# Performance work log

Hardware: AMD Instinct MI355X
Metric: run time of the kernel (lower is better)

Reference implementation:

```python
import jax, jax.numpy as jnp
import numpy as np

NUM_GRAPHS = 64

def _mlp(x, Wa, ba, Wb, bb):
    # 2-layer MLP: Linear -> ReLU -> Linear
    return jnp.maximum(x @ Wa + ba, 0.0) @ Wb + bb

def setup_inputs() -> dict:
    key = jax.random.key(0)
    ks = jax.random.split(key, 16)
    N1, E1, N2, E2 = 20000, 640000, 640000, 1280000
    d_x1, d_x2, d_e2, d_h, d_et, d_out = 32, 32, 16, 64, 32, 32
    inp = {
        'x1': jax.random.normal(ks[0], (N1, d_x1), jnp.float32),
        'x2': jax.random.normal(ks[1], (N2, d_x2), jnp.float32),
        'edge_index1': jax.random.randint(ks[2], (2, E1), 0, N1),
        'edge_index2': jax.random.randint(ks[3], (2, E2), 0, N2),
        'x1_batch': jnp.sort(jax.random.randint(ks[4], (N1,), 0, NUM_GRAPHS)),
        'edge_attr2': jax.random.normal(ks[5], (E2, d_e2), jnp.float32),
        # mlp2 (DGCN edge network): in = d_x2 + d_e2 = 48 -> 64 -> 32
        'W2a': jax.random.normal(ks[6], (d_x2 + d_e2, d_h), jnp.float32) * 0.05,
        'b2a': jnp.zeros((d_h,), jnp.float32),
        'W2b': jax.random.normal(ks[7], (d_h, d_et), jnp.float32) * 0.05,
        'b2b': jnp.zeros((d_et,), jnp.float32),
        # mlp (MOLGCN edge-conditioned network): in = d_x1 + d_et = 64 -> 64 -> 32
        'W1a': jax.random.normal(ks[8], (d_x1 + d_et, d_h), jnp.float32) * 0.05,
        'b1a': jnp.zeros((d_h,), jnp.float32),
        'W1b': jax.random.normal(ks[9], (d_h, d_out), jnp.float32) * 0.05,
        'b1b': jnp.zeros((d_out,), jnp.float32),
    }
    return inp

def reference(x1, x2, edge_index1, edge_index2, x1_batch, edge_attr2,
              W2a, b2a, W2b, b2b, W1a, b1a, W1b, b1b):
    N1, N2 = x1.shape[0], x2.shape[0]
    # --- DGCN over graph 2: message = mlp2([x_src, edge_attr]), sum-aggregate at dst ---
    s2, d2 = edge_index2[0], edge_index2[1]
    msg2 = _mlp(jnp.concatenate([x2[s2], edge_attr2], axis=-1), W2a, b2a, W2b, b2b)  # [E2, d_et]
    e_t = jax.ops.segment_sum(msg2, d2, num_segments=N2)  # [N2, d_et]; N2 == E1 (line graph)
    # --- MOLGCN over graph 1: edge-conditioned message = mlp([x_src, e_t]), sum at dst ---
    s1, d1 = edge_index1[0], edge_index1[1]
    msg1 = _mlp(jnp.concatenate([x1[s1], e_t], axis=-1), W1a, b1a, W1b, b1b)  # [E1, d_out]
    h = jax.ops.segment_sum(msg1, d1, num_segments=N1)  # [N1, d_out]
    # --- global add pool over graphs, then squeeze()/2 ---
    pooled = jax.ops.segment_sum(h, x1_batch, num_segments=NUM_GRAPHS)  # [G, d_out]
    return jnp.squeeze(pooled) / 2.0
```

## Files before the change

kernel.cpp:

```cpp
#include <hip/hip_runtime.h>
#include <hip/hip_bf16.h>


#define NUM_GRAPHS 64
#define CAP 4608
#define CURSTRIDE 16
#define EPB 8192
#define NCVT 2048

typedef __attribute__((ext_vector_type(8))) short bf16x8;
typedef __attribute__((ext_vector_type(4))) float f32x4;

__device__ __forceinline__ unsigned short f2bf(float x) {
    __hip_bfloat16 b = __float2bfloat16(x);
    return *(unsigned short*)&b;
}
__device__ __forceinline__ float bf2f(unsigned int u16) {
    unsigned short us = (unsigned short)u16;
    __hip_bfloat16 b = *(__hip_bfloat16*)&us;
    return __bfloat162float(b);
}
__device__ __forceinline__ unsigned int pack2(float lo, float hi) {
    return (unsigned int)f2bf(lo) | ((unsigned int)f2bf(hi) << 16);
}
__device__ __forceinline__ uint4 cvt8(const float* src) {
    const float4* s4 = (const float4*)src;
    float4 a = s4[0], b = s4[1];
    return make_uint4(pack2(a.x, a.y), pack2(a.z, a.w),
                      pack2(b.x, b.y), pack2(b.z, b.w));
}
__device__ __forceinline__ int swz(int row, int kb) {
    return row * 128 + (kb ^ ((row & 7) << 4));
}


__global__ __launch_bounds__(256) void k_prep0(
    const float* __restrict__ W2a, const float* __restrict__ b2a,
    const float* __restrict__ W2b, const float* __restrict__ b2b,
    const float* __restrict__ W1a, const float* __restrict__ b1a,
    const float* __restrict__ W1b, const float* __restrict__ b1b,
    unsigned char* __restrict__ wpack, int* __restrict__ cur, int ncur)
{
    const int tid = threadIdx.x;
    if (blockIdx.x == 0) {
        unsigned char* img1 = wpack;
        unsigned char* img2 = wpack + 12672;
        for (int i = tid; i < 64 * 64; i += 256) {
            int n = i >> 6, k = i & 63;
            float v1 = (k < 48) ? W2a[k * 64 + n] : 0.0f;
            *(unsigned short*)(img1 + n * 128 + ((2 * k) ^ ((n & 7) << 4))) = f2bf(v1);
            *(unsigned short*)(img2 + n * 128 + ((2 * k) ^ ((n & 7) << 4))) = f2bf(W1a[k * 64 + n]);
        }
        for (int i = tid; i < 32 * 64; i += 256) {
            int n = i >> 6, k = i & 63;
            *(unsigned short*)(img1 + 8192 + n * 128 + ((2 * k) ^ ((n & 7) << 4))) = f2bf(W2b[k * 32 + n]);
            *(unsigned short*)(img2 + 8192 + n * 128 + ((2 * k) ^ ((n & 7) << 4))) = f2bf(W1b[k * 32 + n]);
        }
        if (tid < 64) {
            ((float*)(img1 + 12288))[tid] = b2a[tid];
            ((float*)(img2 + 12288))[tid] = b1a[tid];
        }
        if (tid < 32) {
            ((float*)(img1 + 12544))[tid] = b2b[tid];
            ((float*)(img2 + 12544))[tid] = b1b[tid];
        }
    } else {
        for (int i = tid; i < ncur; i += 256) cur[i] = 0;
    }
}


__global__ __launch_bounds__(256) void k_bscat_cvt(
    const int* __restrict__ ei2, int E2, const int* __restrict__ ei1, int E1,
    int* __restrict__ cur, uint2* __restrict__ mid, int NB2, int NBT, int Etot, int NBB,
    const float* __restrict__ x2, uint4* __restrict__ x2b,
    const float* __restrict__ x1, uint4* __restrict__ x1b,
    const float* __restrict__ ea2, uint4* __restrict__ ea2b,
    long xn2, long xn1, long xne)
{
    __shared__ unsigned int buck[EPB];
    __shared__ int hist[512];
    __shared__ int gbase[512];
    __shared__ int wloc[512];

    const int tid = threadIdx.x;
    if (blockIdx.x >= NBB) {
        const long tot = xn2 + xn1 + xne;
        const long stride = (long)NCVT * 256;
        for (long i = (long)(blockIdx.x - NBB) * 256 + tid; i < tot; i += stride) {
            if (i < xn2) x2b[i] = cvt8(x2 + i * 8);
            else if (i < xn2 + xn1) { long j = i - xn2; x1b[j] = cvt8(x1 + j * 8); }
            else { long j = i - xn2 - xn1; ea2b[j] = cvt8(ea2 + j * 8); }
        }
        return;
    }

    const long start = (long)blockIdx.x * EPB;
    const int nloc = (int)(((long)Etot - start) < EPB ? ((long)Etot - start) : EPB);
    if (nloc <= 0) return;

    for (int i = tid; i < NBT; i += 256) hist[i] = 0;
    __syncthreads();

    for (int k = tid; k < nloc; k += 256) {
        const long i = start + k;
        int b, dlo;
        if (i < E2) {
            int d = ei2[E2 + i]; b = d >> 11; dlo = d & 2047;
        } else {
            int j = (int)(i - E2);
            int d = ei1[E1 + j]; b = NB2 + (d >> 7); dlo = d & 127;
        }
        buck[k] = (unsigned)b | ((unsigned)dlo << 16);
        atomicAdd(&hist[b], 1);
    }
    __syncthreads();

    for (int i = tid; i < NBT; i += 256) {
        const int c = hist[i];
        gbase[i] = (c > 0) ? atomicAdd(&cur[i * CURSTRIDE], c) : 0;
        wloc[i] = 0;
    }
    __syncthreads();

    for (int k = tid; k < nloc; k += 256) {
        const long i = start + k;
        const unsigned bv = buck[k];
        const int b = (int)(bv & 0xffffu), dlo = (int)(bv >> 16);
        int e, s;
        if (i < E2) { e = (int)i; s = ei2[i]; }
        else        { int j = (int)(i - E2); e = j; s = ei1[j]; }
        const int pos = gbase[b] + atomicAdd(&wloc[b], 1);
        if (pos < CAP)
            mid[(size_t)b * CAP + pos] =
                make_uint2((unsigned)e | ((unsigned)dlo << 21), (unsigned)s);
    }
}


__global__ __launch_bounds__(256) void k_csr(
    const int* __restrict__ cur, const uint2* __restrict__ mid,
    uint2* __restrict__ ord, int NB2, int E2)
{
    __shared__ int cnt[2048];
    __shared__ int cnt2[2048];
    __shared__ int red[256];
    __shared__ int wpart[4];
    __shared__ int sCarry;

    const int b = blockIdx.x, tid = threadIdx.x;
    const bool g2 = (b < NB2);
    const int span = g2 ? 2048 : 128;
    const int lo = g2 ? 0 : NB2;
    const int fill = min(cur[b * CURSTRIDE], CAP);

    int part = 0;
    for (int k = lo + tid; k < b; k += 256) part += min(cur[k * CURSTRIDE], CAP);
    red[tid] = part;
    __syncthreads();
    for (int off = 128; off >= 1; off >>= 1) {
        if (tid < off) red[tid] += red[tid + off];
        __syncthreads();
    }
    const int outBase = (g2 ? 0 : E2) + red[0];

    for (int k = tid; k < span; k += 256) cnt[k] = 0;
    __syncthreads();

    const size_t mbase = (size_t)b * CAP;
    for (int i = tid; i < fill; i += 256)
        atomicAdd(&cnt[mid[mbase + i].x >> 21], 1);
    __syncthreads();

    if (tid == 0) sCarry = 0;
    __syncthreads();
    const int lane = tid & 63, wv = tid >> 6;
    for (int c0 = 0; c0 < span; c0 += 256) {
        const int idx = c0 + tid;
        int v = (idx < span) ? cnt[idx] : 0;
        int inc = v;
        #pragma unroll
        for (int off = 1; off < 64; off <<= 1) {
            int nv = __shfl_up(inc, off, 64);
            if (lane >= off) inc += nv;
        }
        if (lane == 63) wpart[wv] = inc;
        __syncthreads();
        int wpre = 0;
        for (int wq = 0; wq < wv; ++wq) wpre += wpart[wq];
        const int excl = sCarry + wpre + inc - v;
        const int tot = wpart[0] + wpart[1] + wpart[2] + wpart[3];
        __syncthreads();
        if (idx < span) cnt[idx] = excl;
        if (tid == 0) sCarry += tot;
        __syncthreads();
    }

    for (int k = tid; k < span; k += 256) cnt2[k] = 0;
    __syncthreads();

    for (int i = tid; i < fill; i += 256) {
        uint2 r = mid[mbase + i];
        const int dl = (int)(r.x >> 21);
        const int rk = atomicAdd(&cnt2[dl], 1);
        ord[outBase + cnt[dl] + rk] = make_uint2(r.x, r.y | ((unsigned)b << 20));
    }
}


__global__ __launch_bounds__(256) void k_msg2_agg(
    const float* __restrict__ x2f, const uint4* __restrict__ x2b,
    const float* __restrict__ ea2, const uint4* __restrict__ ea2b,
    const uint2* __restrict__ ord, const unsigned char* __restrict__ wimg,
    unsigned int* __restrict__ e_t, int E, int use_bf16, int use_ea2b)
{
    __shared__ __align__(16) unsigned char sBuf[32768];
    __shared__ int sdst[257];
    __shared__ int sPrevS;
    __shared__ unsigned long long wmask[4];
    __shared__ int rstart[257];

    const int tid = threadIdx.x;
    const int base = blockIdx.x * 256, p = base + tid;

    int e = 0, s = 0, d = -1;
    if (p < E) {
        uint2 o = ord[p];
        e = (int)(o.x & 0x1FFFFFu); s = (int)(o.y & 0xFFFFFu);
        d = ((int)(o.y >> 20) << 11) + (int)(o.x >> 21);
    }
    sdst[tid] = d;
    if (tid == 0) {
        int dp = -1, dn = -1;
        if (base > 0) {
            uint2 o = ord[base - 1];
            dp = ((int)(o.y >> 20) << 11) + (int)(o.x >> 21);
        }
        if (base + 256 < E) {
            uint2 o = ord[base + 256];
            dn = ((int)(o.y >> 20) << 11) + (int)(o.x >> 21);
        }
        sPrevS = dp; sdst[256] = dn;
    }

    {
        uint4 ch[8];
        if (use_bf16) {
            const uint4* xr = x2b + (size_t)s * 4;
            #pragma unroll
            for (int c = 0; c < 4; ++c) ch[c] = xr[c];
        } else {
            const float4* xs = (const float4*)(x2f + (size_t)s * 32);
            #pragma unroll
            for (int c = 0; c < 4; ++c) {
                float4 a = xs[2 * c], b = xs[2 * c + 1];
                ch[c].x = pack2(a.x, a.y); ch[c].y = pack2(a.z, a.w);
                ch[c].z = pack2(b.x, b.y); ch[c].w = pack2(b.z, b.w);
            }
        }
        if (use_ea2b) {
            ch[4] = ea2b[(size_t)e * 2];
            ch[5] = ea2b[(size_t)e * 2 + 1];
        } else {
            const float4* es = (const float4*)(ea2 + (size_t)e * 16);
            #pragma unroll
            for (int c = 0; c < 2; ++c) {
                float4 a = es[2 * c], b = es[2 * c + 1];
                ch[4 + c].x = pack2(a.x, a.y); ch[4 + c].y = pack2(a.z, a.w);
                ch[4 + c].z = pack2(b.x, b.y); ch[4 + c].w = pack2(b.z, b.w);
            }
        }
        ch[6] = make_uint4(0, 0, 0, 0);
        ch[7] = make_uint4(0, 0, 0, 0);
        #pragma unroll
        for (int c = 0; c < 8; ++c)
            *(uint4*)(sBuf + swz(tid, c * 16)) = ch[c];
    }
    __syncthreads();

    const int lane = tid & 63, wv = tid >> 6;
    const int lr = lane & 15, lk = lane >> 4;
    const int band = wv * 64;
    const unsigned char* gWa = wimg;
    const unsigned char* gWb = wimg + 8192;
    const float* gba = (const float*)(wimg + 12288);
    const float* gbb = (const float*)(wimg + 12544);

    f32x4 accA[4][4];
    #pragma unroll
    for (int n = 0; n < 4; ++n) {
        float bv = gba[n * 16 + lr];
        #pragma unroll
        for (int m = 0; m < 4; ++m) accA[m][n] = (f32x4){bv, bv, bv, bv};
    }
    #pragma unroll
    for (int ks = 0; ks < 2; ++ks) {
        const int kb = ks * 64 + lk * 16;
        bf16x8 af[4], bfr[4];
        #pragma unroll
        for (int m = 0; m < 4; ++m)
            af[m] = *(const bf16x8*)(sBuf + swz(band + m * 16 + lr, kb));
        #pragma unroll
        for (int n = 0; n < 4; ++n) {
            int rw = n * 16 + lr;
            bfr[n] = *(const bf16x8*)(gWa + rw * 128 + (kb ^ ((rw & 7) << 4)));
        }
        #pragma unroll
        for (int m = 0; m < 4; ++m)
            #pragma unroll
            for (int n = 0; n < 4; ++n)
                accA[m][n] = __builtin_amdgcn_mfma_f32_16x16x32_bf16(af[m], bfr[n], accA[m][n], 0, 0, 0);
    }
    #pragma unroll
    for (int m = 0; m < 4; ++m)
        #pragma unroll
        for (int n = 0; n < 4; ++n)
            #pragma unroll
            for (int rr = 0; rr < 4; ++rr) {
                int grow = band + m * 16 + lk * 4 + rr;
                int cb = 2 * (n * 16 + lr);
                *(unsigned short*)(sBuf + swz(grow, cb)) = f2bf(fmaxf(accA[m][n][rr], 0.0f));
            }

    f32x4 accB[4][2];
    #pragma unroll
    for (int n = 0; n < 2; ++n) {
        float bv = gbb[n * 16 + lr];
        #pragma unroll
        for (int m = 0; m < 4; ++m) accB[m][n] = (f32x4){bv, bv, bv, bv};
    }
    #pragma unroll
    for (int ks = 0; ks < 2; ++ks) {
        const int kb = ks * 64 + lk * 16;
        bf16x8 af[4], bfr[2];
        #pragma unroll
        for (int m = 0; m < 4; ++m)
            af[m] = *(const bf16x8*)(sBuf + swz(band + m * 16 + lr, kb));
        #pragma unroll
        for (int n = 0; n < 2; ++n) {
            int rw = n * 16 + lr;
            bfr[n] = *(const bf16x8*)(gWb + rw * 128 + (kb ^ ((rw & 7) << 4)));
        }
        #pragma unroll
        for (int m = 0; m < 4; ++m)
            #pragma unroll
            for (int n = 0; n < 2; ++n)
                accB[m][n] = __builtin_amdgcn_mfma_f32_16x16x32_bf16(af[m], bfr[n], accB[m][n], 0, 0, 0);
    }
    __syncthreads();

    unsigned short* smsg = (unsigned short*)sBuf;
    #pragma unroll
    for (int m = 0; m < 4; ++m)
        #pragma unroll
        for (int n = 0; n < 2; ++n)
            #pragma unroll
            for (int rr = 0; rr < 4; ++rr)
                smsg[(band + m * 16 + lk * 4 + rr) * 33 + n * 16 + lr] = f2bf(accB[m][n][rr]);

    const bool leader = (p < E) && (tid == 0 || sdst[tid - 1] != d);
    wmask[wv] = __ballot(leader);
    __syncthreads();

    int nruns = __popcll(wmask[0]) + __popcll(wmask[1]) + __popcll(wmask[2]) + __popcll(wmask[3]);
    if (leader) {
        int before = __popcll(wmask[wv] & ((1ULL << lane) - 1));
        for (int w = 0; w < wv; ++w) before += __popcll(wmask[w]);
        rstart[before] = tid;
    }
    const int vcnt = (E - base < 256) ? (E - base) : 256;
    if (tid == 0) rstart[nruns] = vcnt;
    __syncthreads();

    const int sPrev = sPrevS;
    const int ntask = nruns * 32;
    for (int task = tid; task < ntask; task += 256) {
        const int run = task >> 5, c = task & 31;
        const int rs = rstart[run], re = rstart[run + 1];
        const int dd = sdst[rs];
        float acc = 0.0f;
        for (int qq = rs; qq < re; ++qq) acc += bf2f(smsg[qq * 33 + c]);
        const bool gs = (rs > 0) || (base == 0) || (sPrev != dd);
        const bool ge = (re < 256) || (sdst[256] != dd);
        if (gs && ge) {
            ((unsigned short*)e_t)[(size_t)dd * 32 + c] = f2bf(acc);
        } else {
            unsigned int* a32 = e_t + (size_t)dd * 16 + (c >> 1);
            const int sh = (c & 1) * 16;
            unsigned int old = *a32;
            while (true) {
                float cur2 = bf2f((old >> sh) & 0xffffu);
                unsigned int nb = f2bf(cur2 + acc);
                unsigned int nv = (old & ~(0xffffu << sh)) | (nb << sh);
                unsigned int prev = atomicCAS(a32, old, nv);
                if (prev == old) break;
                old = prev;
            }
        }
    }
}


__global__ __launch_bounds__(256) void k_msg1_agg(
    const float* __restrict__ x1f, const uint4* __restrict__ x1b,
    const unsigned int* __restrict__ e_t,
    const uint2* __restrict__ ord, const unsigned char* __restrict__ wimg,
    float* __restrict__ h, int E, int NB2, int use_bf16)
{
    __shared__ __align__(16) unsigned char sBuf[32768];
    __shared__ int sdst[257];
    __shared__ int sPrevS;
    __shared__ unsigned long long wmask[4];
    __shared__ int rstart[257];

    const int tid = threadIdx.x;
    const int base = blockIdx.x * 256, p = base + tid;

    int e = 0, s = 0, d = -1;
    if (p < E) {
        uint2 o = ord[p];
        e = (int)(o.x & 0x1FFFFFu); s = (int)(o.y & 0xFFFFFu);
        d = (((int)(o.y >> 20) - NB2) << 7) + (int)(o.x >> 21);
    }
    sdst[tid] = d;
    if (tid == 0) {
        int dp = -1, dn = -1;
        if (base > 0) {
            uint2 o = ord[base - 1];
            dp = (((int)(o.y >> 20) - NB2) << 7) + (int)(o.x >> 21);
        }
        if (base + 256 < E) {
            uint2 o = ord[base + 256];
            dn = (((int)(o.y >> 20) - NB2) << 7) + (int)(o.x >> 21);
        }
        sPrevS = dp; sdst[256] = dn;
    }

    {
        uint4 ch[8];
        if (use_bf16) {
            const uint4* xr = x1b + (size_t)s * 4;
            #pragma unroll
            for (int c = 0; c < 4; ++c) ch[c] = xr[c];
        } else {
            const float4* xs = (const float4*)(x1f + (size_t)s * 32);
            #pragma unroll
            for (int c = 0; c < 4; ++c) {
                float4 a = xs[2 * c], b = xs[2 * c + 1];
                ch[c].x = pack2(a.x, a.y); ch[c].y = pack2(a.z, a.w);
                ch[c].z = pack2(b.x, b.y); ch[c].w = pack2(b.z, b.w);
            }
        }
        const uint4* er = (const uint4*)(e_t + (size_t)e * 16);
        #pragma unroll
        for (int c = 0; c < 4; ++c) ch[4 + c] = er[c];
        #pragma unroll
        for (int c = 0; c < 8; ++c)
            *(uint4*)(sBuf + swz(tid, c * 16)) = ch[c];
    }
    __syncthreads();

    const int lane = tid & 63, wv = tid >> 6;
    const int lr = lane & 15, lk = lane >> 4;
    const int band = wv * 64;
    const unsigned char* gWa = wimg;
    const unsigned char* gWb = wimg + 8192;
    const float* gba = (const float*)(wimg + 12288);
    const float* gbb = (const float*)(wimg + 12544);

    f32x4 accA[4][4];
    #pragma unroll
    for (int n = 0; n < 4; ++n) {
        float bv = gba[n * 16 + lr];
        #pragma unroll
        for (int m = 0; m < 4; ++m) accA[m][n] = (f32x4){bv, bv, bv, bv};
    }
    #pragma unroll
    for (int ks = 0; ks < 2; ++ks) {
        const int kb = ks * 64 + lk * 16;
        bf16x8 af[4], bfr[4];
        #pragma unroll
        for (int m = 0; m < 4; ++m)
            af[m] = *(const bf16x8*)(sBuf + swz(band + m * 16 + lr, kb));
        #pragma unroll
        for (int n = 0; n < 4; ++n) {
            int rw = n * 16 + lr;
            bfr[n] = *(const bf16x8*)(gWa + rw * 128 + (kb ^ ((rw & 7) << 4)));
        }
        #pragma unroll
        for (int m = 0; m < 4; ++m)
            #pragma unroll
            for (int n = 0; n < 4; ++n)
                accA[m][n] = __builtin_amdgcn_mfma_f32_16x16x32_bf16(af[m], bfr[n], accA[m][n], 0, 0, 0);
    }
    #pragma unroll
    for (int m = 0; m < 4; ++m)
        #pragma unroll
        for (int n = 0; n < 4; ++n)
            #pragma unroll
            for (int rr = 0; rr < 4; ++rr) {
                int grow = band + m * 16 + lk * 4 + rr;
                int cb = 2 * (n * 16 + lr);
                *(unsigned short*)(sBuf + swz(grow, cb)) = f2bf(fmaxf(accA[m][n][rr], 0.0f));
            }

    f32x4 accB[4][2];
    #pragma unroll
    for (int n = 0; n < 2; ++n) {
        float bv = gbb[n * 16 + lr];
        #pragma unroll
        for (int m = 0; m < 4; ++m) accB[m][n] = (f32x4){bv, bv, bv, bv};
    }
    #pragma unroll
    for (int ks = 0; ks < 2; ++ks) {
        const int kb = ks * 64 + lk * 16;
        bf16x8 af[4], bfr[2];
        #pragma unroll
        for (int m = 0; m < 4; ++m)
            af[m] = *(const bf16x8*)(sBuf + swz(band + m * 16 + lr, kb));
        #pragma unroll
        for (int n = 0; n < 2; ++n) {
            int rw = n * 16 + lr;
            bfr[n] = *(const bf16x8*)(gWb + rw * 128 + (kb ^ ((rw & 7) << 4)));
        }
        #pragma unroll
        for (int m = 0; m < 4; ++m)
            #pragma unroll
            for (int n = 0; n < 2; ++n)
                accB[m][n] = __builtin_amdgcn_mfma_f32_16x16x32_bf16(af[m], bfr[n], accB[m][n], 0, 0, 0);
    }
    __syncthreads();

    unsigned short* smsg = (unsigned short*)sBuf;
    #pragma unroll
    for (int m = 0; m < 4; ++m)
        #pragma unroll
        for (int n = 0; n < 2; ++n)
            #pragma unroll
            for (int rr = 0; rr < 4; ++rr)
                smsg[(band + m * 16 + lk * 4 + rr) * 33 + n * 16 + lr] = f2bf(accB[m][n][rr]);

    const bool leader = (p < E) && (tid == 0 || sdst[tid - 1] != d);
    wmask[wv] = __ballot(leader);
    __syncthreads();

    int nruns = __popcll(wmask[0]) + __popcll(wmask[1]) + __popcll(wmask[2]) + __popcll(wmask[3]);
    if (leader) {
        int before = __popcll(wmask[wv] & ((1ULL << lane) - 1));
        for (int w = 0; w < wv; ++w) before += __popcll(wmask[w]);
        rstart[before] = tid;
    }
    const int vcnt = (E - base < 256) ? (E - base) : 256;
    if (tid == 0) rstart[nruns] = vcnt;
    __syncthreads();

    const int sPrev = sPrevS;
    const int ntask = nruns * 32;
    for (int task = tid; task < ntask; task += 256) {
        const int run = task >> 5, c = task & 31;
        const int rs = rstart[run], re = rstart[run + 1];
        const int dd = sdst[rs];
        float acc = 0.0f;
        for (int qq = rs; qq < re; ++qq) acc += bf2f(smsg[qq * 33 + c]);
        const bool gs = (rs > 0) || (base == 0) || (sPrev != dd);
        const bool ge = (re < 256) || (sdst[256] != dd);
        if (gs && ge) h[(size_t)dd * 32 + c] = acc;
        else atomicAdd(h + (size_t)dd * 32 + c, acc);
    }
}


__device__ __forceinline__ int lower_bound_i(const int* a, int n, int key) {
    int lo = 0, hi = n;
    while (lo < hi) {
        int mid = (lo + hi) >> 1;
        if (a[mid] < key) lo = mid + 1; else hi = mid;
    }
    return lo;
}

__global__ __launch_bounds__(256) void k_pool(const float* __restrict__ h,
                                              const int* __restrict__ batch,
                                              float* __restrict__ out, int N1) {
    const int g = blockIdx.x;
    const int lo = lower_bound_i(batch, N1, g);
    const int hi = lower_bound_i(batch, N1, g + 1);
    const int tid = threadIdx.x;
    const int c = tid & 31, rg = tid >> 5;
    float acc = 0.0f;
    for (int n = lo + rg; n < hi; n += 8) acc += h[(size_t)n * 32 + c];
    __shared__ float red[256];
    red[tid] = acc;
    __syncthreads();
    for (int off = 128; off >= 32; off >>= 1) {
        if (tid < off) red[tid] += red[tid + off];
        __syncthreads();
    }
    if (tid < 32) out[g * 32 + tid] = red[tid] * 0.5f;
}


extern "C" void kernel_launch(void* const* d_in, const int* in_sizes, int n_in,
                              void* d_out, int out_size, void* d_ws, size_t ws_size,
                              hipStream_t stream) {
    const float* x1  = (const float*)d_in[0];
    const float* x2  = (const float*)d_in[1];
    const int*   ei1 = (const int*)d_in[2];
    const int*   ei2 = (const int*)d_in[3];
    const int*   xb  = (const int*)d_in[4];
    const float* ea2 = (const float*)d_in[5];
    const float* W2a = (const float*)d_in[6];
    const float* b2a = (const float*)d_in[7];
    const float* W2b = (const float*)d_in[8];
    const float* b2b = (const float*)d_in[9];
    const float* W1a = (const float*)d_in[10];
    const float* b1a = (const float*)d_in[11];
    const float* W1b = (const float*)d_in[12];
    const float* b1b = (const float*)d_in[13];

    const int N1 = in_sizes[0] / 32;
    const int E1 = in_sizes[2] / 2;
    const int E2 = in_sizes[3] / 2;
    const int N2 = in_sizes[1] / 32;
    const int Etot = E2 + E1;

    const int NB2 = (N2 + 2047) >> 11;
    const int NB1 = (N1 + 127) >> 7;
    const int NBT = NB2 + NB1;

    const size_t sz_wpack = 25600;
    const size_t sz_cur   = (size_t)NBT * CURSTRIDE * 4;
    const size_t sz_et    = (size_t)N2 * 64;
    const size_t sz_h     = (size_t)N1 * 128;
    const size_t sz_ord   = (size_t)Etot * 8;
    const size_t sz_mid   = (size_t)NBT * CAP * 8;
    const size_t regA     = (sz_mid > sz_et + sz_h) ? sz_mid : (sz_et + sz_h);
    const size_t sz_x2b   = (size_t)N2 * 64;
    const size_t sz_x1b   = (size_t)N1 * 64;
    const size_t sz_ea2b  = (size_t)E2 * 32;
    const size_t need_x   = sz_ord + regA + sz_x2b + sz_x1b + sz_wpack + sz_cur;
    const size_t need_xe  = need_x + sz_ea2b;

    const int use_bf16 = (ws_size >= need_x) ? 1 : 0;
    const int use_ea2b = (ws_size >= need_xe) ? 1 : 0;

    char* w = (char*)d_ws;
    uint2* ord = (uint2*)w;            w += sz_ord;
    char* regionA = w;                 w += regA;
    uint4* x2b = (uint4*)w;            if (use_bf16) w += sz_x2b;
    uint4* x1b = (uint4*)w;            if (use_bf16) w += sz_x1b;
    uint4* ea2b = (uint4*)w;           if (use_ea2b) w += sz_ea2b;
    unsigned char* wpack = (unsigned char*)w;  w += sz_wpack;
    int* cur = (int*)w;

    unsigned int* e_t = (unsigned int*)regionA;
    float* h = (float*)(regionA + sz_et);
    uint2* mid = (uint2*)regionA;

    const int NBB = (Etot + EPB - 1) / EPB;
    const long xn2 = use_bf16 ? (long)N2 * 4 : 0;
    const long xn1 = use_bf16 ? (long)N1 * 4 : 0;
    const long xne = use_ea2b ? (long)E2 * 2 : 0;

    k_prep0<<<2, 256, 0, stream>>>(W2a, b2a, W2b, b2b, W1a, b1a, W1b, b1b,
                                   wpack, cur, NBT * CURSTRIDE);
    k_bscat_cvt<<<NBB + NCVT, 256, 0, stream>>>(
        ei2, E2, ei1, E1, cur, mid, NB2, NBT, Etot, NBB,
        x2, x2b, x1, x1b, ea2, ea2b, xn2, xn1, xne);
    k_csr<<<NBT, 256, 0, stream>>>(cur, mid, ord, NB2, E2);
    hipMemsetAsync(regionA, 0, sz_et + sz_h, stream);
    k_msg2_agg<<<(E2 + 255) / 256, 256, 0, stream>>>(
        x2, x2b, ea2, ea2b, ord, wpack, e_t, E2, use_bf16, use_ea2b);
    k_msg1_agg<<<(E1 + 255) / 256, 256, 0, stream>>>(
        x1, x1b, e_t, ord + E2, wpack + 12672, h, E1, NB2, use_bf16);
    k_pool<<<NUM_GRAPHS, 256, 0, stream>>>(h, xb, (float*)d_out, N1);
}
```

Measured before the change: 262.1 us.

## Carry edge-attr payload through bucket sort and renumber e_t by graph-1 edge rank

```diff
diff --git a/kernel.cpp b/kernel.cpp
--- a/kernel.cpp
+++ b/kernel.cpp
@@ -39,7 +39,8 @@
     const float* __restrict__ W2b, const float* __restrict__ b2b,
     const float* __restrict__ W1a, const float* __restrict__ b1a,
     const float* __restrict__ W1b, const float* __restrict__ b1b,
-    unsigned char* __restrict__ wpack, int* __restrict__ cur, int ncur)
+    unsigned char* __restrict__ wpack, int* __restrict__ cur, int ncur,
+    int* __restrict__ rank1, int nrank)
 {
     const int tid = threadIdx.x;
     if (blockIdx.x == 0) {
@@ -65,18 +66,24 @@
             ((float*)(img2 + 12544))[tid] = b1b[tid];
         }
     } else {
-        for (int i = tid; i < ncur; i += 256) cur[i] = 0;
+        const int Z = ncur + nrank;
+        for (int i = (blockIdx.x - 1) * 256 + tid; i < Z; i += 32 * 256) {
+            if (i < ncur) cur[i] = 0;
+            else rank1[i - ncur] = 0;
+        }
     }
 }
 
 
 __global__ __launch_bounds__(256) void k_bscat_cvt(
     const int* __restrict__ ei2, int E2, const int* __restrict__ ei1, int E1,
-    int* __restrict__ cur, uint2* __restrict__ mid, int NB2, int NBT, int Etot, int NBB,
+    int* __restrict__ cur, uint2* __restrict__ mid8,
+    uint2* __restrict__ mid2_sd, uint4* __restrict__ mid2_pay, uint2* __restrict__ mid1,
+    int NB2, int NBT, int Etot, int NBB,
     const float* __restrict__ x2, uint4* __restrict__ x2b,
     const float* __restrict__ x1, uint4* __restrict__ x1b,
     const float* __restrict__ ea2, uint4* __restrict__ ea2b,
-    long xn2, long xn1, long xne)
+    long xn2, long xn1, long xne, int use_pay)
 {
     __shared__ unsigned int buck[EPB];
     __shared__ int hist[512];
@@ -127,51 +134,33 @@
         const long i = start + k;
         const unsigned bv = buck[k];
         const int b = (int)(bv & 0xffffu), dlo = (int)(bv >> 16);
-        int e, s;
-        if (i < E2) { e = (int)i; s = ei2[i]; }
-        else        { int j = (int)(i - E2); e = j; s = ei1[j]; }
         const int pos = gbase[b] + atomicAdd(&wloc[b], 1);
-        if (pos < CAP)
-            mid[(size_t)b * CAP + pos] =
-                make_uint2((unsigned)e | ((unsigned)dlo << 21), (unsigned)s);
-    }
-}
-
-
-__global__ __launch_bounds__(256) void k_csr(
-    const int* __restrict__ cur, const uint2* __restrict__ mid,
-    uint2* __restrict__ ord, int NB2, int E2)
-{
-    __shared__ int cnt[2048];
-    __shared__ int cnt2[2048];
-    __shared__ int red[256];
+        if (pos >= CAP) continue;
+        if (i < E2) {
+            const int s = ei2[i];
+            if (use_pay) {
+                const size_t idx = (size_t)b * CAP + pos;
+                mid2_sd[idx] = make_uint2((unsigned)s, (unsigned)((b << 11) + dlo));
+                mid2_pay[idx * 2]     = cvt8(ea2 + (size_t)i * 16);
+                mid2_pay[idx * 2 + 1] = cvt8(ea2 + (size_t)i * 16 + 8);
+            } else {
+                mid8[(size_t)b * CAP + pos] =
+                    make_uint2((unsigned)i | ((unsigned)dlo << 21), (unsigned)s);
+            }
+        } else {
+            const int j = (int)(i - E2);
+            const int s = ei1[j];
+            const uint2 rec = make_uint2((unsigned)j | ((unsigned)dlo << 21), (unsigned)s);
+            if (use_pay) mid1[(size_t)(b - NB2) * CAP + pos] = rec;
+            else         mid8[(size_t)b * CAP + pos] = rec;
+        }
+    }
+}
+
+
+__device__ __forceinline__ void lds_excl_scan(int* cnt, int span, int tid) {
     __shared__ int wpart[4];
     __shared__ int sCarry;
-
-    const int b = blockIdx.x, tid = threadIdx.x;
-    const bool g2 = (b < NB2);
-    const int span = g2 ? 2048 : 128;
-    const int lo = g2 ? 0 : NB2;
-    const int fill = min(cur[b * CURSTRIDE], CAP);
-
-    int part = 0;
-    for (int k = lo + tid; k < b; k += 256) part += min(cur[k * CURSTRIDE], CAP);
-    red[tid] = part;
-    __syncthreads();
-    for (int off = 128; off >= 1; off >>= 1) {
-        if (tid < off) red[tid] += red[tid + off];
-        __syncthreads();
-    }
-    const int outBase = (g2 ? 0 : E2) + red[0];
-
-    for (int k = tid; k < span; k += 256) cnt[k] = 0;
-    __syncthreads();
-
-    const size_t mbase = (size_t)b * CAP;
-    for (int i = tid; i < fill; i += 256)
-        atomicAdd(&cnt[mid[mbase + i].x >> 21], 1);
-    __syncthreads();
-
     if (tid == 0) sCarry = 0;
     __syncthreads();
     const int lane = tid & 63, wv = tid >> 6;
@@ -195,10 +184,42 @@
         if (tid == 0) sCarry += tot;
         __syncthreads();
     }
-
+}
+
+
+__global__ __launch_bounds__(256) void k_csr_t1(
+    const int* __restrict__ cur, const uint2* __restrict__ mid,
+    uint2* __restrict__ ord, int NB2, int E2)
+{
+    __shared__ int cnt[2048];
+    __shared__ int cnt2[2048];
+    __shared__ int red[256];
+
+    const int b = blockIdx.x, tid = threadIdx.x;
+    const bool g2 = (b < NB2);
+    const int span = g2 ? 2048 : 128;
+    const int lo = g2 ? 0 : NB2;
+    const int fill = min(cur[b * CURSTRIDE], CAP);
+
+    int part = 0;
+    for (int k = lo + tid; k < b; k += 256) part += min(cur[k * CURSTRIDE], CAP);
+    red[tid] = part;
+    __syncthreads();
+    for (int off = 128; off >= 1; off >>= 1) {
+        if (tid < off) red[tid] += red[tid + off];
+        __syncthreads();
+    }
+    const int outBase = (g2 ? 0 : E2) + red[0];
+
+    for (int k = tid; k < span; k += 256) cnt[k] = 0;
+    __syncthreads();
+    const size_t mbase = (size_t)b * CAP;
+    for (int i = tid; i < fill; i += 256)
+        atomicAdd(&cnt[mid[mbase + i].x >> 21], 1);
+    __syncthreads();
+    lds_excl_scan(cnt, span, tid);
     for (int k = tid; k < span; k += 256) cnt2[k] = 0;
     __syncthreads();
-
     for (int i = tid; i < fill; i += 256) {
         uint2 r = mid[mbase + i];
         const int dl = (int)(r.x >> 21);
@@ -208,39 +229,128 @@
 }
 
 
+__global__ __launch_bounds__(256) void k_csr1(
+    const int* __restrict__ cur, const uint2* __restrict__ mid1,
+    uint2* __restrict__ ord1, int* __restrict__ rank1, int NB2)
+{
+    __shared__ int cnt[128];
+    __shared__ int cnt2[128];
+    __shared__ int red[256];
+
+    const int bl = blockIdx.x, tid = threadIdx.x;
+    const int bg = NB2 + bl;
+    const int fill = min(cur[bg * CURSTRIDE], CAP);
+
+    int part = 0;
+    for (int k = NB2 + tid; k < bg; k += 256) part += min(cur[k * CURSTRIDE], CAP);
+    red[tid] = part;
+    __syncthreads();
+    for (int off = 128; off >= 1; off >>= 1) {
+        if (tid < off) red[tid] += red[tid + off];
+        __syncthreads();
+    }
+    const int outBase = red[0];
+
+    if (tid < 128) { cnt[tid] = 0; cnt2[tid] = 0; }
+    __syncthreads();
+    const size_t mbase = (size_t)bl * CAP;
+    for (int i = tid; i < fill; i += 256)
+        atomicAdd(&cnt[mid1[mbase + i].x >> 21], 1);
+    __syncthreads();
+    lds_excl_scan(cnt, 128, tid);
+    __syncthreads();
+    for (int i = tid; i < fill; i += 256) {
+        uint2 r = mid1[mbase + i];
+        const int dl = (int)(r.x >> 21);
+        const int rk = atomicAdd(&cnt2[dl], 1);
+        const int o = outBase + cnt[dl] + rk;
+        ord1[o] = make_uint2(r.x, r.y | ((unsigned)bg << 20));
+        rank1[r.x & 0x1FFFFFu] = o;
+    }
+}
+
+
+__global__ __launch_bounds__(256) void k_csr2(
+    const int* __restrict__ cur,
+    const uint2* __restrict__ mid2_sd, const uint4* __restrict__ mid2_pay,
+    uint2* __restrict__ ord2_sd, uint4* __restrict__ ord2_pay,
+    const int* __restrict__ rank1, int E1)
+{
+    __shared__ int cnt[2048];
+    __shared__ int cnt2[2048];
+    __shared__ int red[256];
+
+    const int b = blockIdx.x, tid = threadIdx.x;
+    const int node0 = b << 11;
+    const int fill = min(cur[b * CURSTRIDE], CAP);
+
+    int part = 0;
+    for (int k = tid; k < b; k += 256) part += min(cur[k * CURSTRIDE], CAP);
+    red[tid] = part;
+    __syncthreads();
+    for (int off = 128; off >= 1; off >>= 1) {
+        if (tid < off) red[tid] += red[tid + off];
+        __syncthreads();
+    }
+    const int outBase = red[0];
+
+    for (int k = tid; k < 2048; k += 256) { cnt[k] = 0; cnt2[k] = 0; }
+    __syncthreads();
+    const size_t mbase = (size_t)b * CAP;
+    for (int i = tid; i < fill; i += 256)
+        atomicAdd(&cnt[(int)mid2_sd[mbase + i].y - node0], 1);
+    __syncthreads();
+    lds_excl_scan(cnt, 2048, tid);
+    __syncthreads();
+    for (int i = tid; i < fill; i += 256) {
+        uint2 sd = mid2_sd[mbase + i];
+        const int dl = (int)sd.y - node0;
+        const int rk = atomicAdd(&cnt2[dl], 1);
+        const int o = outBase + cnt[dl] + rk;
+        unsigned rp = (unsigned)rank1[sd.y];
+        if (rp >= (unsigned)E1) rp = 0;
+        ord2_sd[o] = make_uint2(sd.x, rp);
+        ord2_pay[(size_t)o * 2]     = mid2_pay[(mbase + i) * 2];
+        ord2_pay[(size_t)o * 2 + 1] = mid2_pay[(mbase + i) * 2 + 1];
+    }
+}
+
+
 __global__ __launch_bounds__(256) void k_msg2_agg(
     const float* __restrict__ x2f, const uint4* __restrict__ x2b,
     const float* __restrict__ ea2, const uint4* __restrict__ ea2b,
-    const uint2* __restrict__ ord, const unsigned char* __restrict__ wimg,
-    unsigned int* __restrict__ e_t, int E, int use_bf16, int use_ea2b)
+    const uint2* __restrict__ ordp, const uint2* __restrict__ sd2,
+    const uint4* __restrict__ pay2,
+    const unsigned char* __restrict__ wimg,
+    unsigned int* __restrict__ e_t, int E,
+    int use_bf16, int use_ea2b, int use_pay)
 {
     __shared__ __align__(16) unsigned char sBuf[32768];
-    __shared__ int sdst[257];
-    __shared__ int sPrevS;
-    __shared__ unsigned long long wmask[4];
-    __shared__ int rstart[257];
+    unsigned short* smsg = (unsigned short*)sBuf;
+    int* sdst = (int*)(sBuf + 16896);
+    int* rstart = (int*)(sBuf + 16896 + 1032);
+    unsigned long long* wmaskS = (unsigned long long*)(sBuf + 16896 + 1032 + 1032);
 
     const int tid = threadIdx.x;
     const int base = blockIdx.x * 256, p = base + tid;
 
-    int e = 0, s = 0, d = -1;
-    if (p < E) {
-        uint2 o = ord[p];
-        e = (int)(o.x & 0x1FFFFFu); s = (int)(o.y & 0xFFFFFu);
-        d = ((int)(o.y >> 20) << 11) + (int)(o.x >> 21);
-    }
-    sdst[tid] = d;
-    if (tid == 0) {
-        int dp = -1, dn = -1;
-        if (base > 0) {
-            uint2 o = ord[base - 1];
-            dp = ((int)(o.y >> 20) << 11) + (int)(o.x >> 21);
-        }
-        if (base + 256 < E) {
-            uint2 o = ord[base + 256];
-            dn = ((int)(o.y >> 20) << 11) + (int)(o.x >> 21);
-        }
-        sPrevS = dp; sdst[256] = dn;
+    int e = 0, s = 0, d = -1, dp_ = -1, dn_ = -1;
+    if (use_pay) {
+        if (p < E) { uint2 o = sd2[p]; s = (int)o.x; d = (int)o.y; }
+        if (tid == 0) {
+            if (base > 0) dp_ = (int)sd2[base - 1].y;
+            if (base + 256 < E) dn_ = (int)sd2[base + 256].y;
+        }
+    } else {
+        if (p < E) {
+            uint2 o = ordp[p];
+            e = (int)(o.x & 0x1FFFFFu); s = (int)(o.y & 0xFFFFFu);
+            d = ((int)(o.y >> 20) << 11) + (int)(o.x >> 21);
+        }
+        if (tid == 0) {
+            if (base > 0) { uint2 o = ordp[base - 1]; dp_ = ((int)(o.y >> 20) << 11) + (int)(o.x >> 21); }
+            if (base + 256 < E) { uint2 o = ordp[base + 256]; dn_ = ((int)(o.y >> 20) << 11) + (int)(o.x >> 21); }
+        }
     }
 
     {
@@ -258,7 +368,15 @@
                 ch[c].z = pack2(b.x, b.y); ch[c].w = pack2(b.z, b.w);
             }
         }
-        if (use_ea2b) {
+        if (use_pay) {
+            if (p < E) {
+                ch[4] = pay2[(size_t)p * 2];
+                ch[5] = pay2[(size_t)p * 2 + 1];
+            } else {
+                ch[4] = make_uint4(0, 0, 0, 0);
+                ch[5] = make_uint4(0, 0, 0, 0);
+            }
+        } else if (use_ea2b) {
             ch[4] = ea2b[(size_t)e * 2];
             ch[5] = ea2b[(size_t)e * 2 + 1];
         } else {
@@ -349,7 +467,6 @@
     }
     __syncthreads();
 
-    unsigned short* smsg = (unsigned short*)sBuf;
     #pragma unroll
     for (int m = 0; m < 4; ++m)
         #pragma unroll
@@ -357,22 +474,25 @@
             #pragma unroll
             for (int rr = 0; rr < 4; ++rr)
                 smsg[(band + m * 16 + lk * 4 + rr) * 33 + n * 16 + lr] = f2bf(accB[m][n][rr]);
+    sdst[tid] = d;
+    if (tid == 0) { sdst[256] = dn_; sdst[257] = dp_; }
+    __syncthreads();
 
     const bool leader = (p < E) && (tid == 0 || sdst[tid - 1] != d);
-    wmask[wv] = __ballot(leader);
-    __syncthreads();
-
-    int nruns = __popcll(wmask[0]) + __popcll(wmask[1]) + __popcll(wmask[2]) + __popcll(wmask[3]);
+    wmaskS[wv] = __ballot(leader);
+    __syncthreads();
+
+    int nruns = __popcll(wmaskS[0]) + __popcll(wmaskS[1]) + __popcll(wmaskS[2]) + __popcll(wmaskS[3]);
     if (leader) {
-        int before = __popcll(wmask[wv] & ((1ULL << lane) - 1));
-        for (int w = 0; w < wv; ++w) before += __popcll(wmask[w]);
+        int before = __popcll(wmaskS[wv] & ((1ULL << lane) - 1));
+        for (int w = 0; w < wv; ++w) before += __popcll(wmaskS[w]);
         rstart[before] = tid;
     }
     const int vcnt = (E - base < 256) ? (E - base) : 256;
     if (tid == 0) rstart[nruns] = vcnt;
     __syncthreads();
 
-    const int sPrev = sPrevS;
+    const int sPrev = sdst[257];
     const int ntask = nruns * 32;
     for (int task = tid; task < ntask; task += 256) {
         const int run = task >> 5, c = task & 31;
@@ -404,36 +524,27 @@
 __global__ __launch_bounds__(256) void k_msg1_agg(
     const float* __restrict__ x1f, const uint4* __restrict__ x1b,
     const unsigned int* __restrict__ e_t,
-    const uint2* __restrict__ ord, const unsigned char* __restrict__ wimg,
-    float* __restrict__ h, int E, int NB2, int use_bf16)
+    const uint2* __restrict__ ordp, const unsigned char* __restrict__ wimg,
+    float* __restrict__ h, int E, int NB2, int use_bf16, int use_pay)
 {
     __shared__ __align__(16) unsigned char sBuf[32768];
-    __shared__ int sdst[257];
-    __shared__ int sPrevS;
-    __shared__ unsigned long long wmask[4];
-    __shared__ int rstart[257];
+    unsigned short* smsg = (unsigned short*)sBuf;
+    int* sdst = (int*)(sBuf + 16896);
+    int* rstart = (int*)(sBuf + 16896 + 1032);
+    unsigned long long* wmaskS = (unsigned long long*)(sBuf + 16896 + 1032 + 1032);
 
     const int tid = threadIdx.x;
     const int base = blockIdx.x * 256, p = base + tid;
 
-    int e = 0, s = 0, d = -1;
+    int e = 0, s = 0, d = -1, dp_ = -1, dn_ = -1;
     if (p < E) {
-        uint2 o = ord[p];
+        uint2 o = ordp[p];
         e = (int)(o.x & 0x1FFFFFu); s = (int)(o.y & 0xFFFFFu);
         d = (((int)(o.y >> 20) - NB2) << 7) + (int)(o.x >> 21);
     }
-    sdst[tid] = d;
     if (tid == 0) {
-        int dp = -1, dn = -1;
-        if (base > 0) {
-            uint2 o = ord[base - 1];
-            dp = (((int)(o.y >> 20) - NB2) << 7) + (int)(o.x >> 21);
-        }
-        if (base + 256 < E) {
-            uint2 o = ord[base + 256];
-            dn = (((int)(o.y >> 20) - NB2) << 7) + (int)(o.x >> 21);
-        }
-        sPrevS = dp; sdst[256] = dn;
+        if (base > 0) { uint2 o = ordp[base - 1]; dp_ = (((int)(o.y >> 20) - NB2) << 7) + (int)(o.x >> 21); }
+        if (base + 256 < E) { uint2 o = ordp[base + 256]; dn_ = (((int)(o.y >> 20) - NB2) << 7) + (int)(o.x >> 21); }
     }
 
     {
@@ -451,7 +562,8 @@
                 ch[c].z = pack2(b.x, b.y); ch[c].w = pack2(b.z, b.w);
             }
         }
-        const uint4* er = (const uint4*)(e_t + (size_t)e * 16);
+        const size_t erow = use_pay ? (size_t)((p < E) ? p : 0) : (size_t)e;
+        const uint4* er = (const uint4*)(e_t + erow * 16);
         #pragma unroll
         for (int c = 0; c < 4; ++c) ch[4 + c] = er[c];
         #pragma unroll
@@ -531,7 +643,6 @@
     }
     __syncthreads();
 
-    unsigned short* smsg = (unsigned short*)sBuf;
     #pragma unroll
     for (int m = 0; m < 4; ++m)
         #pragma unroll
@@ -539,22 +650,25 @@
             #pragma unroll
             for (int rr = 0; rr < 4; ++rr)
                 smsg[(band + m * 16 + lk * 4 + rr) * 33 + n * 16 + lr] = f2bf(accB[m][n][rr]);
+    sdst[tid] = d;
+    if (tid == 0) { sdst[256] = dn_; sdst[257] = dp_; }
+    __syncthreads();
 
     const bool leader = (p < E) && (tid == 0 || sdst[tid - 1] != d);
-    wmask[wv] = __ballot(leader);
-    __syncthreads();
-
-    int nruns = __popcll(wmask[0]) + __popcll(wmask[1]) + __popcll(wmask[2]) + __popcll(wmask[3]);
+    wmaskS[wv] = __ballot(leader);
+    __syncthreads();
+
+    int nruns = __popcll(wmaskS[0]) + __popcll(wmaskS[1]) + __popcll(wmaskS[2]) + __popcll(wmaskS[3]);
     if (leader) {
-        int before = __popcll(wmask[wv] & ((1ULL << lane) - 1));
-        for (int w = 0; w < wv; ++w) before += __popcll(wmask[w]);
+        int before = __popcll(wmaskS[wv] & ((1ULL << lane) - 1));
+        for (int w = 0; w < wv; ++w) before += __popcll(wmaskS[w]);
         rstart[before] = tid;
     }
     const int vcnt = (E - base < 256) ? (E - base) : 256;
     if (tid == 0) rstart[nruns] = vcnt;
     __syncthreads();
 
-    const int sPrev = sPrevS;
+    const int sPrev = sdst[257];
     const int ntask = nruns * 32;
     for (int task = tid; task < ntask; task += 256) {
         const int run = task >> 5, c = task & 31;
@@ -632,46 +746,89 @@
     const size_t sz_cur   = (size_t)NBT * CURSTRIDE * 4;
     const size_t sz_et    = (size_t)N2 * 64;
     const size_t sz_h     = (size_t)N1 * 128;
-    const size_t sz_ord   = (size_t)Etot * 8;
-    const size_t sz_mid   = (size_t)NBT * CAP * 8;
-    const size_t regA     = (sz_mid > sz_et + sz_h) ? sz_mid : (sz_et + sz_h);
     const size_t sz_x2b   = (size_t)N2 * 64;
     const size_t sz_x1b   = (size_t)N1 * 64;
+
+    const size_t sz_ord8  = (size_t)Etot * 8;
+    const size_t sz_mid8  = (size_t)NBT * CAP * 8;
+    const size_t regA_t1  = (sz_mid8 > sz_et + sz_h) ? sz_mid8 : (sz_et + sz_h);
     const size_t sz_ea2b  = (size_t)E2 * 32;
-    const size_t need_x   = sz_ord + regA + sz_x2b + sz_x1b + sz_wpack + sz_cur;
+    const size_t need_x   = sz_ord8 + regA_t1 + sz_x2b + sz_x1b + sz_wpack + sz_cur;
     const size_t need_xe  = need_x + sz_ea2b;
 
-    const int use_bf16 = (ws_size >= need_x) ? 1 : 0;
-    const int use_ea2b = (ws_size >= need_xe) ? 1 : 0;
+    const size_t sz_o2sd  = (size_t)E2 * 8;
+    const size_t sz_o2pay = (size_t)E2 * 32;
+    const size_t sz_ord1  = (size_t)E1 * 8;
+    const size_t sz_rank  = (size_t)N2 * 4;
+    const size_t sz_m2sd  = (size_t)NB2 * CAP * 8;
+    const size_t sz_m2pay = (size_t)NB2 * CAP * 32;
+    const size_t sz_m1    = (size_t)NB1 * CAP * 8;
+    const size_t midsum   = sz_m2sd + sz_m2pay + sz_m1;
+    const size_t regA_t2  = (midsum > sz_et + sz_h) ? midsum : (sz_et + sz_h);
+    const size_t need_pay = sz_o2sd + sz_o2pay + sz_ord1 + sz_rank + regA_t2
+                          + sz_x2b + sz_x1b + sz_wpack + sz_cur;
+
+    const int use_pay  = (ws_size >= need_pay) ? 1 : 0;
+    const int use_bf16 = use_pay ? 1 : ((ws_size >= need_x) ? 1 : 0);
+    const int use_ea2b = use_pay ? 0 : ((ws_size >= need_xe) ? 1 : 0);
 
     char* w = (char*)d_ws;
-    uint2* ord = (uint2*)w;            w += sz_ord;
-    char* regionA = w;                 w += regA;
-    uint4* x2b = (uint4*)w;            if (use_bf16) w += sz_x2b;
-    uint4* x1b = (uint4*)w;            if (use_bf16) w += sz_x1b;
-    uint4* ea2b = (uint4*)w;           if (use_ea2b) w += sz_ea2b;
-    unsigned char* wpack = (unsigned char*)w;  w += sz_wpack;
-    int* cur = (int*)w;
-
+    uint2* ord8 = nullptr; uint2* o2sd = nullptr; uint4* o2pay = nullptr;
+    uint2* ord1 = nullptr; int* rank1 = nullptr;
+    uint2* mid8 = nullptr; uint2* m2sd = nullptr; uint4* m2pay = nullptr; uint2* m1 = nullptr;
+    uint4 *x2b, *x1b, *ea2bp = nullptr;
+    unsigned char* wpack; int* cur;
+    char* regionA;
+
+    if (use_pay) {
+        o2sd  = (uint2*)w;  w += sz_o2sd;
+        o2pay = (uint4*)w;  w += sz_o2pay;
+        ord1  = (uint2*)w;  w += sz_ord1;
+        rank1 = (int*)w;    w += sz_rank;
+        regionA = w;        w += regA_t2;
+        x2b = (uint4*)w;    w += sz_x2b;
+        x1b = (uint4*)w;    w += sz_x1b;
+        wpack = (unsigned char*)w; w += sz_wpack;
+        cur = (int*)w;
+        m2sd  = (uint2*)regionA;
+        m2pay = (uint4*)(regionA + sz_m2sd);
+        m1    = (uint2*)(regionA + sz_m2sd + sz_m2pay);
+    } else {
+        ord8 = (uint2*)w;   w += sz_ord8;
+        regionA = w;        w += regA_t1;
+        x2b = (uint4*)w;    if (use_bf16) w += sz_x2b;
+        x1b = (uint4*)w;    if (use_bf16) w += sz_x1b;
+        ea2bp = (uint4*)w;  if (use_ea2b) w += sz_ea2b;
+        wpack = (unsigned char*)w; w += sz_wpack;
+        cur = (int*)w;
+        mid8 = (uint2*)regionA;
+    }
     unsigned int* e_t = (unsigned int*)regionA;
     float* h = (float*)(regionA + sz_et);
-    uint2* mid = (uint2*)regionA;
 
     const int NBB = (Etot + EPB - 1) / EPB;
     const long xn2 = use_bf16 ? (long)N2 * 4 : 0;
     const long xn1 = use_bf16 ? (long)N1 * 4 : 0;
     const long xne = use_ea2b ? (long)E2 * 2 : 0;
 
-    k_prep0<<<2, 256, 0, stream>>>(W2a, b2a, W2b, b2b, W1a, b1a, W1b, b1b,
-                                   wpack, cur, NBT * CURSTRIDE);
+    k_prep0<<<33, 256, 0, stream>>>(W2a, b2a, W2b, b2b, W1a, b1a, W1b, b1b,
+                                    wpack, cur, NBT * CURSTRIDE,
+                                    rank1, use_pay ? N2 : 0);
     k_bscat_cvt<<<NBB + NCVT, 256, 0, stream>>>(
-        ei2, E2, ei1, E1, cur, mid, NB2, NBT, Etot, NBB,
-        x2, x2b, x1, x1b, ea2, ea2b, xn2, xn1, xne);
-    k_csr<<<NBT, 256, 0, stream>>>(cur, mid, ord, NB2, E2);
+        ei2, E2, ei1, E1, cur, mid8, m2sd, m2pay, m1,
+        NB2, NBT, Etot, NBB, x2, x2b, x1, x1b, ea2, ea2bp, xn2, xn1, xne, use_pay);
+    if (use_pay) {
+        k_csr1<<<NB1, 256, 0, stream>>>(cur, m1, ord1, rank1, NB2);
+        k_csr2<<<NB2, 256, 0, stream>>>(cur, m2sd, m2pay, o2sd, o2pay, rank1, E1);
+    } else {
+        k_csr_t1<<<NBT, 256, 0, stream>>>(cur, mid8, ord8, NB2, E2);
+    }
     hipMemsetAsync(regionA, 0, sz_et + sz_h, stream);
     k_msg2_agg<<<(E2 + 255) / 256, 256, 0, stream>>>(
-        x2, x2b, ea2, ea2b, ord, wpack, e_t, E2, use_bf16, use_ea2b);
+        x2, x2b, ea2, ea2bp, ord8, o2sd, o2pay, wpack, e_t, E2,
+        use_bf16, use_ea2b, use_pay);
     k_msg1_agg<<<(E1 + 255) / 256, 256, 0, stream>>>(
-        x1, x1b, e_t, ord + E2, wpack + 12672, h, E1, NB2, use_bf16);
+        x1, x1b, e_t, use_pay ? ord1 : (ord8 + E2), wpack + 12672, h, E1, NB2,
+        use_bf16, use_pay);
     k_pool<<<NUM_GRAPHS, 256, 0, stream>>>(h, xb, (float*)d_out, N1);
 }
```

Result: slower. 319.2 us (+21.8%).
